# Optimization experiments

Hardware: AMD Instinct MI355X
Metric: run time of the kernel (lower is better)

## Reference

```python
import jax, jax.numpy as jnp
import numpy as np
import math


def setup_inputs() -> dict:
    key = jax.random.key(0)
    ks = jax.random.split(key, 5)
    B, C, E = 4, 2048, 1024
    max_len = 2048
    s = 1.0 / math.sqrt(E)
    return {
        "x": jax.random.normal(ks[0], (B, C, E), dtype=jnp.float32),
        "W_q": jax.random.normal(ks[1], (E, E), dtype=jnp.float32) * s,
        "W_k": jax.random.normal(ks[2], (E, E), dtype=jnp.float32) * s,
        "W_v": jax.random.normal(ks[3], (E, E), dtype=jnp.float32) * s,
        "rel_bias": jax.random.normal(ks[4], (2 * max_len - 1, 1), dtype=jnp.float32),
        "max_len": max_len,
    }


def reference(x, W_q, W_k, W_v, rel_bias, max_len):
    B, C, E = x.shape
    # nn.Linear(bias=False): y = x @ W.T
    Q = jnp.einsum("bce,fe->bcf", x, W_q)
    K = jnp.einsum("bce,fe->bcf", x, W_k)
    V = jnp.einsum("bce,fe->bcf", x, W_v)
    scores = jnp.einsum("bqe,bke->bqk", Q, K) / math.sqrt(E)
    pos = jnp.arange(C)
    rel_dist = jnp.clip(pos[None, :] - pos[:, None] + (max_len - 1), 0, 2 * max_len - 2)
    bias = rel_bias[rel_dist, 0]  # [C, C]
    scores = scores + bias[None, :, :]
    weights = jax.nn.softmax(scores, axis=-1)
    out = jnp.einsum("bqk,bke->bqe", weights, V)
    return out, weights
```

## Files before the change

### kernel.cpp

```cpp
#include <hip/hip_runtime.h>
#include <hip/hip_bf16.h>
#include <math.h>

typedef __attribute__((ext_vector_type(8))) short short8;
typedef __attribute__((ext_vector_type(4))) short short4v;
typedef __attribute__((ext_vector_type(4))) float f32x4;

static __device__ __forceinline__ short f2bf(float f) {
  union { float f; unsigned u; } x;
  x.f = f;
  unsigned r = x.u + 0x7fffu + ((x.u >> 16) & 1u);
  return (short)(r >> 16);
}

#define GLD16(g, l)                                                   \
  __builtin_amdgcn_global_load_lds(                                   \
      (const __attribute__((address_space(1))) void*)(g),             \
      (__attribute__((address_space(3))) void*)(l), 16, 0, 0)
#define BAR() asm volatile("s_barrier" ::: "memory")
#define VMCNT6() asm volatile("s_waitcnt vmcnt(6)" ::: "memory")
#define VMCNT0() asm volatile("s_waitcnt vmcnt(0)" ::: "memory")

__global__ __launch_bounds__(256) void cvt_f32_bf16(const float* __restrict__ in,
                                                    short* __restrict__ out, int n8) {
  int i = blockIdx.x * 256 + threadIdx.x;
  if (i >= n8) return;
  const float4* p = (const float4*)in + (size_t)i * 2;
  float4 a = p[0], b = p[1];
  short8 o;
  o[0] = f2bf(a.x); o[1] = f2bf(a.y); o[2] = f2bf(a.z); o[3] = f2bf(a.w);
  o[4] = f2bf(b.x); o[5] = f2bf(b.y); o[6] = f2bf(b.z); o[7] = f2bf(b.w);
  *((short8*)out + i) = o;
}

template <int MODE>
__global__ __launch_bounds__(512) void gemm3b(
    const short* __restrict__ A, const short* __restrict__ Bt,
    void* __restrict__ C0, void* __restrict__ C1, void* __restrict__ C2,
    const float* __restrict__ rel_bias,
    int N, int K, long aZ, long bZ, long cZ, int Cdim, float scale, int ml) {
  __shared__ short sA[3][256 * 64];
  __shared__ short sB[3][128 * 64];
  const int tid = threadIdx.x, lane = tid & 63, wid = tid >> 6;
  const int z = blockIdx.z;
  const short* Az = A + (size_t)z * aZ;
  const short* Bz = Bt + (size_t)z * bZ;
  const int brow = blockIdx.x * 256, bcol = blockIdx.y * 128;
  const int wr = wid >> 2, wc = wid & 3;
  const int lrow = lane & 15, kg = lane >> 4;
  const int l8 = lane >> 3, lm8 = lane & 7;
  const int scol = (lm8 ^ l8) * 8;

  const short* aS[2][2];
  int aD[2][2];
#pragma unroll
  for (int h = 0; h < 2; ++h)
#pragma unroll
    for (int j = 0; j < 2; ++j) {
      int c = wid * 2 + j;
      int rb = c * 8 + (c >= 8 ? 64 : 0) + h * 64;
      aS[h][j] = Az + (size_t)(brow + rb + l8) * K + scol;
      aD[h][j] = rb * 64;
    }
  const short* bS[2];
  int bD[2];
#pragma unroll
  for (int h = 0; h < 2; ++h) {
    int rb = wid * 8 + h * 64;
    bS[h] = Bz + (size_t)(bcol + rb + l8) * K + scol;
    bD[h] = rb * 64;
  }

  const int sks0 = ((0 + kg) ^ (lrow & 7)) * 8;
  const int sks1 = ((4 + kg) ^ (lrow & 7)) * 8;
  const int aR = (wr * 128 + lrow) * 64;
  const int bR = (wc * 32 + lrow) * 64;

  short8 a[4][2], b[2][2];
  f32x4 acc[8][2] = {};

  short *pa0 = &sA[0][0], *pa1 = &sA[1][0], *pa2 = &sA[2][0];
  short *pb0 = &sB[0][0], *pb1 = &sB[1][0], *pb2 = &sB[2][0];

#define STG_A(PA, H, T)                                          \
  do {                                                           \
    GLD16(aS[H][0] + (size_t)(T) * 64, (PA) + aD[H][0]);         \
    GLD16(aS[H][1] + (size_t)(T) * 64, (PA) + aD[H][1]);         \
  } while (0)
#define STG_B(PB, H, T) GLD16(bS[H] + (size_t)(T) * 64, (PB) + bD[H])
#define RD_A(PA, MH)                                                          \
  do {                                                                        \
    _Pragma("unroll") for (int mq = 0; mq < 4; ++mq) {                        \
      a[mq][0] = *(const short8*)&(PA)[aR + (MH)*4096 + mq * 1024 + sks0];    \
      a[mq][1] = *(const short8*)&(PA)[aR + (MH)*4096 + mq * 1024 + sks1];    \
    }                                                                         \
  } while (0)
#define RD_B(PB)                                                   \
  do {                                                             \
    _Pragma("unroll") for (int nq = 0; nq < 2; ++nq) {             \
      b[nq][0] = *(const short8*)&(PB)[bR + nq * 1024 + sks0];     \
      b[nq][1] = *(const short8*)&(PB)[bR + nq * 1024 + sks1];     \
    }                                                              \
  } while (0)
#define MFMA16(MH)                                                            \
  do {                                                                        \
    __builtin_amdgcn_s_setprio(1);                                            \
    _Pragma("unroll") for (int mq = 0; mq < 4; ++mq)                          \
        _Pragma("unroll") for (int nq = 0; nq < 2; ++nq) {                    \
      acc[(MH)*4 + mq][nq] = __builtin_amdgcn_mfma_f32_16x16x32_bf16(         \
          a[mq][0], b[nq][0], acc[(MH)*4 + mq][nq], 0, 0, 0);                 \
      acc[(MH)*4 + mq][nq] = __builtin_amdgcn_mfma_f32_16x16x32_bf16(         \
          a[mq][1], b[nq][1], acc[(MH)*4 + mq][nq], 0, 0, 0);                 \
    }                                                                         \
    __builtin_amdgcn_s_setprio(0);                                            \
  } while (0)

  STG_A(pa0, 0, 0); STG_B(pb0, 0, 0); STG_A(pa0, 1, 0); STG_B(pb0, 1, 0);
  STG_A(pa1, 0, 1); STG_B(pb1, 0, 1); STG_A(pa1, 1, 1); STG_B(pb1, 1, 1);
  VMCNT6();
  BAR();

  const int NT = K >> 6;
  for (int t = 0; t < NT - 2; ++t) {
    RD_A(pa0, 0); RD_B(pb0);
    STG_A(pa2, 0, t + 2); STG_B(pb2, 0, t + 2);
    BAR();
    MFMA16(0);
    BAR();
    RD_A(pa0, 1);
    STG_A(pa2, 1, t + 2); STG_B(pb2, 1, t + 2);
    VMCNT6();
    BAR();
    MFMA16(1);
    BAR();
    short* q;
    q = pa0; pa0 = pa1; pa1 = pa2; pa2 = q;
    q = pb0; pb0 = pb1; pb1 = pb2; pb2 = q;
  }
  RD_A(pa0, 0); RD_B(pb0);
  BAR(); MFMA16(0); BAR();
  RD_A(pa0, 1);
  VMCNT0();
  BAR(); MFMA16(1); BAR();
  RD_A(pa1, 0); RD_B(pb1);
  BAR(); MFMA16(0); BAR();
  RD_A(pa1, 1);
  BAR(); MFMA16(1);

#pragma unroll
  for (int m = 0; m < 8; ++m) {
#pragma unroll
    for (int n = 0; n < 2; ++n) {
#pragma unroll
      for (int r = 0; r < 4; ++r) {
        float v = acc[m][n][r];
        int gr = brow + wr * 128 + m * 16 + kg * 4 + r;
        int gc = bcol + wc * 32 + n * 16 + lrow;
        if constexpr (MODE == 2) {
          int idx = gc - gr + (ml - 1);
          idx = min(max(idx, 0), 2 * ml - 2);
          ((float*)C0 + (size_t)z * cZ)[(size_t)gr * N + gc] =
              v * scale + rel_bias[idx];
        } else if constexpr (MODE == 3) {
          ((float*)C0 + (size_t)z * cZ)[(size_t)gr * N + gc] = v;
        } else {
          int s = gc >> 10, cc = gc & 1023;
          if (s == 0) {
            ((short*)C0)[(size_t)gr * 1024 + cc] = f2bf(v);
          } else if (s == 1) {
            ((short*)C1)[(size_t)gr * 1024 + cc] = f2bf(v);
          } else {
            int b_ = gr / Cdim, c_ = gr % Cdim;
            ((short*)C2)[((size_t)b_ * 1024 + cc) * Cdim + c_] = f2bf(v);
          }
        }
      }
    }
  }
#undef STG_A
#undef STG_B
#undef RD_A
#undef RD_B
#undef MFMA16
}

__global__ __launch_bounds__(256) void softmax_rows(float* __restrict__ w,
                                                    short* __restrict__ wb, int Cd) {
  const size_t row = blockIdx.x;
  float4* p = (float4*)(w + row * (size_t)Cd);
  const int tid = threadIdx.x;
  float4 v0 = p[tid];
  float4 v1 = p[tid + 256];
  float mx = fmaxf(fmaxf(fmaxf(v0.x, v0.y), fmaxf(v0.z, v0.w)),
                   fmaxf(fmaxf(v1.x, v1.y), fmaxf(v1.z, v1.w)));
#pragma unroll
  for (int o = 32; o; o >>= 1) mx = fmaxf(mx, __shfl_xor(mx, o));
  __shared__ float red[8];
  const int wv = tid >> 6;
  if ((tid & 63) == 0) red[wv] = mx;
  __syncthreads();
  mx = fmaxf(fmaxf(red[0], red[1]), fmaxf(red[2], red[3]));
  v0.x = __expf(v0.x - mx); v0.y = __expf(v0.y - mx);
  v0.z = __expf(v0.z - mx); v0.w = __expf(v0.w - mx);
  v1.x = __expf(v1.x - mx); v1.y = __expf(v1.y - mx);
  v1.z = __expf(v1.z - mx); v1.w = __expf(v1.w - mx);
  float s = v0.x + v0.y + v0.z + v0.w + v1.x + v1.y + v1.z + v1.w;
#pragma unroll
  for (int o = 32; o; o >>= 1) s += __shfl_xor(s, o);
  if ((tid & 63) == 0) red[4 + wv] = s;
  __syncthreads();
  s = red[4] + red[5] + red[6] + red[7];
  float inv = 1.0f / s;
  v0.x *= inv; v0.y *= inv; v0.z *= inv; v0.w *= inv;
  v1.x *= inv; v1.y *= inv; v1.z *= inv; v1.w *= inv;
  p[tid] = v0;
  p[tid + 256] = v1;
  short4v b0, b1;
  b0[0] = f2bf(v0.x); b0[1] = f2bf(v0.y); b0[2] = f2bf(v0.z); b0[3] = f2bf(v0.w);
  b1[0] = f2bf(v1.x); b1[1] = f2bf(v1.y); b1[2] = f2bf(v1.z); b1[3] = f2bf(v1.w);
  short* wrow = wb + row * (size_t)Cd;
  *(short4v*)&wrow[tid * 4] = b0;
  *(short4v*)&wrow[1024 + tid * 4] = b1;
}

extern "C" void kernel_launch(void* const* d_in, const int* in_sizes, int n_in,
                              void* d_out, int out_size, void* d_ws, size_t ws_size,
                              hipStream_t stream) {
  const float* x = (const float*)d_in[0];
  const float* Wq = (const float*)d_in[1];
  const float* Wk = (const float*)d_in[2];
  const float* Wv = (const float*)d_in[3];
  const float* rb = (const float*)d_in[4];

  const int E = 1024;
  const int Mt = in_sizes[0] / E;
  const int Cd = out_size / Mt - E;
  const int B = Mt / Cd;
  const int ml = (in_sizes[4] + 1) / 2;
  const float scale = 1.0f / sqrtf((float)E);

  short* xb = (short*)d_ws;
  short* wqb = xb + (size_t)Mt * E;
  short* wkb = wqb + (size_t)E * E;
  short* wvb = wkb + (size_t)E * E;
  short* Qb = wvb + (size_t)E * E;
  short* Kb = Qb + (size_t)Mt * E;
  short* Vt = Kb + (size_t)Mt * E;
  short* wbf = Qb;

  float* outp = (float*)d_out;
  float* wts = outp + (size_t)Mt * E;

  cvt_f32_bf16<<<(Mt * E) / 2048, 256, 0, stream>>>(x, xb, (Mt * E) / 8);
  cvt_f32_bf16<<<(E * E) / 2048, 256, 0, stream>>>(Wq, wqb, (E * E) / 8);
  cvt_f32_bf16<<<(E * E) / 2048, 256, 0, stream>>>(Wk, wkb, (E * E) / 8);
  cvt_f32_bf16<<<(E * E) / 2048, 256, 0, stream>>>(Wv, wvb, (E * E) / 8);

  dim3 blk(512);
  gemm3b<4><<<dim3(Mt / 256, 3 * E / 128, 1), blk, 0, stream>>>(
      xb, wqb, Qb, Kb, Vt, nullptr, 3 * E, E, 0, 0, 0, Cd, 0.f, ml);
  gemm3b<2><<<dim3(Cd / 256, Cd / 128, B), blk, 0, stream>>>(
      Qb, Kb, wts, nullptr, nullptr, rb, Cd, E, (long)Cd * E, (long)Cd * E,
      (long)Cd * Cd, Cd, scale, ml);
  softmax_rows<<<Mt, 256, 0, stream>>>(wts, wbf, Cd);
  gemm3b<3><<<dim3(Cd / 256, E / 128, B), blk, 0, stream>>>(
      wbf, Vt, outp, nullptr, nullptr, nullptr, E, Cd, (long)Cd * Cd,
      (long)E * Cd, (long)Cd * E, Cd, 0.f, ml);
}
```

Baseline: 209.2 us.

## Enlarge GEMM tiles to 256x256 with K=32 four-stage LDS pipeline

Replaces the 256x128 tile, K=64, three-buffer GEMM with a 256x256 tile, K=32 slice, four-buffer pipeline. Each wave now computes a 128x64 sub-tile of 32 accumulators. This raises MFMA work per LDS read and per global load, and the deeper ring keeps more loads in flight. The larger tile doubles accumulator registers and halves the grid, which may hurt occupancy and wave balance, especially for the smaller output GEMM.

```diff
diff --git a/kernel.cpp b/kernel.cpp
--- a/kernel.cpp
+++ b/kernel.cpp
@@ -18,7 +18,8 @@
       (const __attribute__((address_space(1))) void*)(g),             \
       (__attribute__((address_space(3))) void*)(l), 16, 0, 0)
 #define BAR() asm volatile("s_barrier" ::: "memory")
-#define VMCNT6() asm volatile("s_waitcnt vmcnt(6)" ::: "memory")
+#define VMCNT8() asm volatile("s_waitcnt vmcnt(8)" ::: "memory")
+#define VMCNT4() asm volatile("s_waitcnt vmcnt(4)" ::: "memory")
 #define VMCNT0() asm volatile("s_waitcnt vmcnt(0)" ::: "memory")
 
 __global__ __launch_bounds__(256) void cvt_f32_bf16(const float* __restrict__ in,
@@ -34,128 +35,118 @@
 }
 
 template <int MODE>
-__global__ __launch_bounds__(512) void gemm3b(
+__global__ __launch_bounds__(512) void gemm4b(
     const short* __restrict__ A, const short* __restrict__ Bt,
     void* __restrict__ C0, void* __restrict__ C1, void* __restrict__ C2,
     const float* __restrict__ rel_bias,
     int N, int K, long aZ, long bZ, long cZ, int Cdim, float scale, int ml) {
-  __shared__ short sA[3][256 * 64];
-  __shared__ short sB[3][128 * 64];
+  __shared__ short sA[4][256 * 32];
+  __shared__ short sB[4][256 * 32];
   const int tid = threadIdx.x, lane = tid & 63, wid = tid >> 6;
   const int z = blockIdx.z;
   const short* Az = A + (size_t)z * aZ;
   const short* Bz = Bt + (size_t)z * bZ;
-  const int brow = blockIdx.x * 256, bcol = blockIdx.y * 128;
+  const int brow = blockIdx.x * 256, bcol = blockIdx.y * 256;
   const int wr = wid >> 2, wc = wid & 3;
   const int lrow = lane & 15, kg = lane >> 4;
-  const int l8 = lane >> 3, lm8 = lane & 7;
-  const int scol = (lm8 ^ l8) * 8;
-
-  const short* aS[2][2];
-  int aD[2][2];
-#pragma unroll
-  for (int h = 0; h < 2; ++h)
-#pragma unroll
-    for (int j = 0; j < 2; ++j) {
-      int c = wid * 2 + j;
-      int rb = c * 8 + (c >= 8 ? 64 : 0) + h * 64;
-      aS[h][j] = Az + (size_t)(brow + rb + l8) * K + scol;
-      aD[h][j] = rb * 64;
-    }
-  const short* bS[2];
-  int bD[2];
-#pragma unroll
-  for (int h = 0; h < 2; ++h) {
-    int rb = wid * 8 + h * 64;
-    bS[h] = Bz + (size_t)(bcol + rb + l8) * K + scol;
-    bD[h] = rb * 64;
-  }
-
-  const int sks0 = ((0 + kg) ^ (lrow & 7)) * 8;
-  const int sks1 = ((4 + kg) ^ (lrow & 7)) * 8;
-  const int aR = (wr * 128 + lrow) * 64;
-  const int bR = (wc * 32 + lrow) * 64;
-
-  short8 a[4][2], b[2][2];
-  f32x4 acc[8][2] = {};
-
-  short *pa0 = &sA[0][0], *pa1 = &sA[1][0], *pa2 = &sA[2][0];
-  short *pb0 = &sB[0][0], *pb1 = &sB[1][0], *pb2 = &sB[2][0];
-
-#define STG_A(PA, H, T)                                          \
-  do {                                                           \
-    GLD16(aS[H][0] + (size_t)(T) * 64, (PA) + aD[H][0]);         \
-    GLD16(aS[H][1] + (size_t)(T) * 64, (PA) + aD[H][1]);         \
-  } while (0)
-#define STG_B(PB, H, T) GLD16(bS[H] + (size_t)(T) * 64, (PB) + bD[H])
-#define RD_A(PA, MH)                                                          \
-  do {                                                                        \
-    _Pragma("unroll") for (int mq = 0; mq < 4; ++mq) {                        \
-      a[mq][0] = *(const short8*)&(PA)[aR + (MH)*4096 + mq * 1024 + sks0];    \
-      a[mq][1] = *(const short8*)&(PA)[aR + (MH)*4096 + mq * 1024 + sks1];    \
-    }                                                                         \
-  } while (0)
-#define RD_B(PB)                                                   \
-  do {                                                             \
-    _Pragma("unroll") for (int nq = 0; nq < 2; ++nq) {             \
-      b[nq][0] = *(const short8*)&(PB)[bR + nq * 1024 + sks0];     \
-      b[nq][1] = *(const short8*)&(PB)[bR + nq * 1024 + sks1];     \
-    }                                                              \
+
+  const int srow = wid * 16 + (lane >> 2);
+  const int scol = ((lane & 3) ^ ((lane >> 2) & 3)) * 8;
+  const short* aSrc0 = Az + (size_t)(brow + srow) * K + scol;
+  const short* aSrc1 = Az + (size_t)(brow + 128 + srow) * K + scol;
+  const short* bSrc0 = Bz + (size_t)(bcol + srow) * K + scol;
+  const short* bSrc1 = Bz + (size_t)(bcol + 128 + srow) * K + scol;
+  const int d0 = wid * 512, d1 = 4096 + wid * 512;
+
+  const int kOff = (kg ^ (lrow & 3)) * 8;
+  const int aBase = (wr * 128 + lrow) * 32 + kOff;
+  const int bBase = (wc * 64 + lrow) * 32 + kOff;
+
+  short8 a[4], b[4];
+  f32x4 acc[8][4] = {};
+
+  short *pa0 = &sA[0][0], *pa1 = &sA[1][0], *pa2 = &sA[2][0], *pa3 = &sA[3][0];
+  short *pb0 = &sB[0][0], *pb1 = &sB[1][0], *pb2 = &sB[2][0], *pb3 = &sB[3][0];
+
+#define STG_A(P, T)                                   \
+  do {                                                \
+    GLD16(aSrc0 + (size_t)(T) * 32, (P) + d0);        \
+    GLD16(aSrc1 + (size_t)(T) * 32, (P) + d1);        \
+  } while (0)
+#define STG_B(P, T)                                   \
+  do {                                                \
+    GLD16(bSrc0 + (size_t)(T) * 32, (P) + d0);        \
+    GLD16(bSrc1 + (size_t)(T) * 32, (P) + d1);        \
+  } while (0)
+#define RD_A(P, MH)                                                 \
+  do {                                                              \
+    _Pragma("unroll") for (int m = 0; m < 4; ++m)                   \
+        a[m] = *(const short8*)&(P)[aBase + ((MH)*4 + m) * 512];    \
+  } while (0)
+#define RD_B(P)                                                     \
+  do {                                                              \
+    _Pragma("unroll") for (int n = 0; n < 4; ++n)                   \
+        b[n] = *(const short8*)&(P)[bBase + n * 512];               \
   } while (0)
 #define MFMA16(MH)                                                            \
   do {                                                                        \
     __builtin_amdgcn_s_setprio(1);                                            \
-    _Pragma("unroll") for (int mq = 0; mq < 4; ++mq)                          \
-        _Pragma("unroll") for (int nq = 0; nq < 2; ++nq) {                    \
-      acc[(MH)*4 + mq][nq] = __builtin_amdgcn_mfma_f32_16x16x32_bf16(         \
-          a[mq][0], b[nq][0], acc[(MH)*4 + mq][nq], 0, 0, 0);                 \
-      acc[(MH)*4 + mq][nq] = __builtin_amdgcn_mfma_f32_16x16x32_bf16(         \
-          a[mq][1], b[nq][1], acc[(MH)*4 + mq][nq], 0, 0, 0);                 \
-    }                                                                         \
+    _Pragma("unroll") for (int m = 0; m < 4; ++m)                             \
+        _Pragma("unroll") for (int n = 0; n < 4; ++n)                         \
+            acc[(MH)*4 + m][n] = __builtin_amdgcn_mfma_f32_16x16x32_bf16(     \
+                a[m], b[n], acc[(MH)*4 + m][n], 0, 0, 0);                     \
     __builtin_amdgcn_s_setprio(0);                                            \
   } while (0)
-
-  STG_A(pa0, 0, 0); STG_B(pb0, 0, 0); STG_A(pa0, 1, 0); STG_B(pb0, 1, 0);
-  STG_A(pa1, 0, 1); STG_B(pb1, 0, 1); STG_A(pa1, 1, 1); STG_B(pb1, 1, 1);
-  VMCNT6();
+#define ROT()                                                    \
+  do {                                                           \
+    short* q;                                                    \
+    q = pa0; pa0 = pa1; pa1 = pa2; pa2 = pa3; pa3 = q;           \
+    q = pb0; pb0 = pb1; pb1 = pb2; pb2 = pb3; pb3 = q;           \
+  } while (0)
+
+  STG_A(pa0, 0); STG_B(pb0, 0);
+  STG_A(pa1, 1); STG_B(pb1, 1);
+  STG_A(pa2, 2); STG_B(pb2, 2);
+  VMCNT8();
   BAR();
 
-  const int NT = K >> 6;
-  for (int t = 0; t < NT - 2; ++t) {
+  const int NT = K >> 5;
+  for (int t = 0; t < NT - 3; ++t) {
     RD_A(pa0, 0); RD_B(pb0);
-    STG_A(pa2, 0, t + 2); STG_B(pb2, 0, t + 2);
-    BAR();
-    MFMA16(0);
-    BAR();
+    STG_A(pa3, t + 3);
+    BAR(); MFMA16(0); BAR();
     RD_A(pa0, 1);
-    STG_A(pa2, 1, t + 2); STG_B(pb2, 1, t + 2);
-    VMCNT6();
-    BAR();
-    MFMA16(1);
-    BAR();
-    short* q;
-    q = pa0; pa0 = pa1; pa1 = pa2; pa2 = q;
-    q = pb0; pb0 = pb1; pb1 = pb2; pb2 = q;
+    STG_B(pb3, t + 3);
+    VMCNT8();
+    BAR(); MFMA16(1); BAR();
+    ROT();
   }
+  RD_A(pa0, 0); RD_B(pb0);
+  BAR(); MFMA16(0); BAR();
+  RD_A(pa0, 1);
+  VMCNT4();
+  BAR(); MFMA16(1); BAR();
+  ROT();
   RD_A(pa0, 0); RD_B(pb0);
   BAR(); MFMA16(0); BAR();
   RD_A(pa0, 1);
   VMCNT0();
   BAR(); MFMA16(1); BAR();
-  RD_A(pa1, 0); RD_B(pb1);
+  ROT();
+  RD_A(pa0, 0); RD_B(pb0);
   BAR(); MFMA16(0); BAR();
-  RD_A(pa1, 1);
+  RD_A(pa0, 1);
   BAR(); MFMA16(1);
 
 #pragma unroll
   for (int m = 0; m < 8; ++m) {
 #pragma unroll
-    for (int n = 0; n < 2; ++n) {
+    for (int n = 0; n < 4; ++n) {
 #pragma unroll
       for (int r = 0; r < 4; ++r) {
         float v = acc[m][n][r];
         int gr = brow + wr * 128 + m * 16 + kg * 4 + r;
-        int gc = bcol + wc * 32 + n * 16 + lrow;
+        int gc = bcol + wc * 64 + n * 16 + lrow;
         if constexpr (MODE == 2) {
           int idx = gc - gr + (ml - 1);
           idx = min(max(idx, 0), 2 * ml - 2);
@@ -182,6 +173,7 @@
 #undef RD_A
 #undef RD_B
 #undef MFMA16
+#undef ROT
 }
 
 __global__ __launch_bounds__(256) void softmax_rows(float* __restrict__ w,
@@ -257,13 +249,13 @@
   cvt_f32_bf16<<<(E * E) / 2048, 256, 0, stream>>>(Wv, wvb, (E * E) / 8);
 
   dim3 blk(512);
-  gemm3b<4><<<dim3(Mt / 256, 3 * E / 128, 1), blk, 0, stream>>>(
+  gemm4b<4><<<dim3(Mt / 256, 3 * E / 256, 1), blk, 0, stream>>>(
       xb, wqb, Qb, Kb, Vt, nullptr, 3 * E, E, 0, 0, 0, Cd, 0.f, ml);
-  gemm3b<2><<<dim3(Cd / 256, Cd / 128, B), blk, 0, stream>>>(
+  gemm4b<2><<<dim3(Cd / 256, Cd / 256, B), blk, 0, stream>>>(
       Qb, Kb, wts, nullptr, nullptr, rb, Cd, E, (long)Cd * E, (long)Cd * E,
       (long)Cd * Cd, Cd, scale, ml);
   softmax_rows<<<Mt, 256, 0, stream>>>(wts, wbf, Cd);
-  gemm3b<3><<<dim3(Cd / 256, E / 128, B), blk, 0, stream>>>(
+  gemm4b<3><<<dim3(Cd / 256, E / 256, B), blk, 0, stream>>>(
       wbf, Vt, outp, nullptr, nullptr, nullptr, E, Cd, (long)Cd * Cd,
       (long)E * Cd, (long)Cd * E, Cd, 0.f, ml);
 }
```

After: 251.8 us. +20.4%, slower.

## Enlarge GEMM tiles to 256x256 with double-buffered eight-phase pipeline

Applied to the files above, without the earlier changes.

The GEMM kernel moves from 256x128 output tiles with a triple-buffered 64-deep K pipeline to 256x256 tiles with double-buffered LDS. The K loop processes two 64-wide slices per iteration in eight MFMA phases, interleaving global-to-LDS loads with finer lgkmcnt/vmcnt waits. The goal is higher arithmetic intensity per loaded byte and fewer blocks. The cost is a larger accumulator register footprint (128 floats per lane), more barriers, and fewer blocks, which can hurt occupancy or wave-count balance on the output GEMM (E/256 columns).

```diff
diff --git a/kernel.cpp b/kernel.cpp
--- a/kernel.cpp
+++ b/kernel.cpp
@@ -18,8 +18,10 @@
       (const __attribute__((address_space(1))) void*)(g),             \
       (__attribute__((address_space(3))) void*)(l), 16, 0, 0)
 #define BAR() asm volatile("s_barrier" ::: "memory")
-#define VMCNT6() asm volatile("s_waitcnt vmcnt(6)" ::: "memory")
-#define VMCNT0() asm volatile("s_waitcnt vmcnt(0)" ::: "memory")
+#define LGKM0() asm volatile("s_waitcnt lgkmcnt(0)" ::: "memory")
+#define LGKM8() asm volatile("s_waitcnt lgkmcnt(8)" ::: "memory")
+#define VMC4() asm volatile("s_waitcnt vmcnt(4)" ::: "memory")
+#define VMC0() asm volatile("s_waitcnt vmcnt(0)" ::: "memory")
 
 __global__ __launch_bounds__(256) void cvt_f32_bf16(const float* __restrict__ in,
                                                     short* __restrict__ out, int n8) {
@@ -34,128 +36,149 @@
 }
 
 template <int MODE>
-__global__ __launch_bounds__(512) void gemm3b(
+__global__ __launch_bounds__(512) void gemm8p(
     const short* __restrict__ A, const short* __restrict__ Bt,
     void* __restrict__ C0, void* __restrict__ C1, void* __restrict__ C2,
     const float* __restrict__ rel_bias,
     int N, int K, long aZ, long bZ, long cZ, int Cdim, float scale, int ml) {
-  __shared__ short sA[3][256 * 64];
-  __shared__ short sB[3][128 * 64];
+  __shared__ short sA[2][16384];
+  __shared__ short sB[2][16384];
   const int tid = threadIdx.x, lane = tid & 63, wid = tid >> 6;
   const int z = blockIdx.z;
   const short* Az = A + (size_t)z * aZ;
   const short* Bz = Bt + (size_t)z * bZ;
-  const int brow = blockIdx.x * 256, bcol = blockIdx.y * 128;
+  const int brow = blockIdx.x * 256, bcol = blockIdx.y * 256;
   const int wr = wid >> 2, wc = wid & 3;
   const int lrow = lane & 15, kg = lane >> 4;
-  const int l8 = lane >> 3, lm8 = lane & 7;
-  const int scol = (lm8 ^ l8) * 8;
-
+
+  const int t8 = tid >> 3, t7 = tid & 7;
+  const int logslot = t7 ^ (t8 & 7);
   const short* aS[2][2];
-  int aD[2][2];
+  const short* bS[2][2];
 #pragma unroll
   for (int h = 0; h < 2; ++h)
 #pragma unroll
     for (int j = 0; j < 2; ++j) {
-      int c = wid * 2 + j;
-      int rb = c * 8 + (c >= 8 ? 64 : 0) + h * 64;
-      aS[h][j] = Az + (size_t)(brow + rb + l8) * K + scol;
-      aD[h][j] = rb * 64;
+      aS[h][j] = Az + (size_t)(brow + h * 128 + j * 64 + t8) * K + logslot * 8;
+      bS[h][j] = Bz + (size_t)(bcol + h * 128 + j * 64 + t8) * K + logslot * 8;
     }
-  const short* bS[2];
-  int bD[2];
-#pragma unroll
-  for (int h = 0; h < 2; ++h) {
-    int rb = wid * 8 + h * 64;
-    bS[h] = Bz + (size_t)(bcol + rb + l8) * K + scol;
-    bD[h] = rb * 64;
-  }
-
-  const int sks0 = ((0 + kg) ^ (lrow & 7)) * 8;
-  const int sks1 = ((4 + kg) ^ (lrow & 7)) * 8;
-  const int aR = (wr * 128 + lrow) * 64;
-  const int bR = (wc * 32 + lrow) * 64;
-
-  short8 a[4][2], b[2][2];
-  f32x4 acc[8][2] = {};
-
-  short *pa0 = &sA[0][0], *pa1 = &sA[1][0], *pa2 = &sA[2][0];
-  short *pb0 = &sB[0][0], *pb1 = &sB[1][0], *pb2 = &sB[2][0];
-
-#define STG_A(PA, H, T)                                          \
-  do {                                                           \
-    GLD16(aS[H][0] + (size_t)(T) * 64, (PA) + aD[H][0]);         \
-    GLD16(aS[H][1] + (size_t)(T) * 64, (PA) + aD[H][1]);         \
-  } while (0)
-#define STG_B(PB, H, T) GLD16(bS[H] + (size_t)(T) * 64, (PB) + bD[H])
-#define RD_A(PA, MH)                                                          \
-  do {                                                                        \
-    _Pragma("unroll") for (int mq = 0; mq < 4; ++mq) {                        \
-      a[mq][0] = *(const short8*)&(PA)[aR + (MH)*4096 + mq * 1024 + sks0];    \
-      a[mq][1] = *(const short8*)&(PA)[aR + (MH)*4096 + mq * 1024 + sks1];    \
+
+  const int kOff0 = ((0 + kg) ^ (lrow & 7)) * 8;
+  const int kOff1 = ((4 + kg) ^ (lrow & 7)) * 8;
+  const int rA = (wr * 128 + lrow) * 64;
+  const int rB = (wc * 64 + lrow) * 64;
+
+  short* const A0 = &sA[0][0];
+  short* const A1 = &sA[1][0];
+  short* const B0 = &sB[0][0];
+  short* const B1 = &sB[1][0];
+
+  short8 av[2][2], bv[4][2];
+  f32x4 acc[8][4] = {};
+
+#define STG_A(BUF, H, T)                                                      \
+  do {                                                                        \
+    GLD16(aS[H][0] + (size_t)(T) * 64, &sA[BUF][(H) * 8192 + wid * 512]);     \
+    GLD16(aS[H][1] + (size_t)(T) * 64, &sA[BUF][(H) * 8192 + 4096 + wid * 512]); \
+  } while (0)
+#define STG_B(BUF, H, T)                                                      \
+  do {                                                                        \
+    GLD16(bS[H][0] + (size_t)(T) * 64, &sB[BUF][(H) * 8192 + wid * 512]);     \
+    GLD16(bS[H][1] + (size_t)(T) * 64, &sB[BUF][(H) * 8192 + 4096 + wid * 512]); \
+  } while (0)
+#define RD_APAIR(P, PP)                                                       \
+  do {                                                                        \
+    av[0][0] = *(const short8*)&(P)[rA + ((PP) * 2 + 0) * 1024 + kOff0];      \
+    av[0][1] = *(const short8*)&(P)[rA + ((PP) * 2 + 0) * 1024 + kOff1];      \
+    av[1][0] = *(const short8*)&(P)[rA + ((PP) * 2 + 1) * 1024 + kOff0];      \
+    av[1][1] = *(const short8*)&(P)[rA + ((PP) * 2 + 1) * 1024 + kOff1];      \
+  } while (0)
+#define RD_BALL(P)                                                            \
+  do {                                                                        \
+    _Pragma("unroll") for (int n = 0; n < 4; ++n) {                           \
+      bv[n][0] = *(const short8*)&(P)[rB + n * 1024 + kOff0];                 \
+      bv[n][1] = *(const short8*)&(P)[rB + n * 1024 + kOff1];                 \
     }                                                                         \
   } while (0)
-#define RD_B(PB)                                                   \
-  do {                                                             \
-    _Pragma("unroll") for (int nq = 0; nq < 2; ++nq) {             \
-      b[nq][0] = *(const short8*)&(PB)[bR + nq * 1024 + sks0];     \
-      b[nq][1] = *(const short8*)&(PB)[bR + nq * 1024 + sks1];     \
-    }                                                              \
-  } while (0)
-#define MFMA16(MH)                                                            \
+#define MFMA_PH(PP)                                                           \
   do {                                                                        \
     __builtin_amdgcn_s_setprio(1);                                            \
-    _Pragma("unroll") for (int mq = 0; mq < 4; ++mq)                          \
-        _Pragma("unroll") for (int nq = 0; nq < 2; ++nq) {                    \
-      acc[(MH)*4 + mq][nq] = __builtin_amdgcn_mfma_f32_16x16x32_bf16(         \
-          a[mq][0], b[nq][0], acc[(MH)*4 + mq][nq], 0, 0, 0);                 \
-      acc[(MH)*4 + mq][nq] = __builtin_amdgcn_mfma_f32_16x16x32_bf16(         \
-          a[mq][1], b[nq][1], acc[(MH)*4 + mq][nq], 0, 0, 0);                 \
+    _Pragma("unroll") for (int mp = 0; mp < 2; ++mp)                          \
+        _Pragma("unroll") for (int n = 0; n < 4; ++n) {                       \
+      acc[(PP) * 2 + mp][n] = __builtin_amdgcn_mfma_f32_16x16x32_bf16(        \
+          av[mp][0], bv[n][0], acc[(PP) * 2 + mp][n], 0, 0, 0);               \
+      acc[(PP) * 2 + mp][n] = __builtin_amdgcn_mfma_f32_16x16x32_bf16(        \
+          av[mp][1], bv[n][1], acc[(PP) * 2 + mp][n], 0, 0, 0);               \
     }                                                                         \
     __builtin_amdgcn_s_setprio(0);                                            \
   } while (0)
 
-  STG_A(pa0, 0, 0); STG_B(pb0, 0, 0); STG_A(pa0, 1, 0); STG_B(pb0, 1, 0);
-  STG_A(pa1, 0, 1); STG_B(pb1, 0, 1); STG_A(pa1, 1, 1); STG_B(pb1, 1, 1);
-  VMCNT6();
+  STG_A(0, 0, 0); STG_A(0, 1, 0); STG_B(0, 0, 0); STG_B(0, 1, 0);
+  STG_B(1, 0, 1); STG_B(1, 1, 1);
+  VMC4();
   BAR();
 
-  const int NT = K >> 6;
-  for (int t = 0; t < NT - 2; ++t) {
-    RD_A(pa0, 0); RD_B(pb0);
-    STG_A(pa2, 0, t + 2); STG_B(pb2, 0, t + 2);
+  const int NIT = K >> 7;
+  for (int i = 0; i < NIT - 1; ++i) {
+    const int tU = 2 * i + 1, tV = 2 * i + 2, tW = 2 * i + 3;
+    RD_BALL(B0); RD_APAIR(A0, 0);
+    STG_A(1, 0, tU);
+    LGKM8();
+    BAR(); LGKM0(); MFMA_PH(0); BAR();
+    RD_APAIR(A0, 1); STG_A(1, 1, tU);
+    BAR(); LGKM0(); MFMA_PH(1); BAR();
+    RD_APAIR(A0, 2); STG_B(0, 0, tV);
+    BAR(); LGKM0(); MFMA_PH(2); BAR();
+    RD_APAIR(A0, 3); STG_B(0, 1, tV);
+    BAR(); LGKM0(); MFMA_PH(3);
+    VMC4();
     BAR();
-    MFMA16(0);
+    RD_BALL(B1); RD_APAIR(A1, 0);
+    STG_A(0, 0, tV);
+    LGKM8();
+    BAR(); LGKM0(); MFMA_PH(0); BAR();
+    RD_APAIR(A1, 1); STG_A(0, 1, tV);
+    BAR(); LGKM0(); MFMA_PH(1); BAR();
+    RD_APAIR(A1, 2); STG_B(1, 0, tW);
+    BAR(); LGKM0(); MFMA_PH(2); BAR();
+    RD_APAIR(A1, 3); STG_B(1, 1, tW);
+    BAR(); LGKM0(); MFMA_PH(3);
+    VMC4();
     BAR();
-    RD_A(pa0, 1);
-    STG_A(pa2, 1, t + 2); STG_B(pb2, 1, t + 2);
-    VMCNT6();
+  }
+  {
+    const int tU = 2 * NIT - 1;
+    RD_BALL(B0); RD_APAIR(A0, 0);
+    STG_A(1, 0, tU);
+    LGKM8();
+    BAR(); LGKM0(); MFMA_PH(0); BAR();
+    RD_APAIR(A0, 1); STG_A(1, 1, tU);
+    BAR(); LGKM0(); MFMA_PH(1); BAR();
+    RD_APAIR(A0, 2);
+    BAR(); LGKM0(); MFMA_PH(2); BAR();
+    RD_APAIR(A0, 3);
+    BAR(); LGKM0(); MFMA_PH(3);
+    VMC0();
     BAR();
-    MFMA16(1);
-    BAR();
-    short* q;
-    q = pa0; pa0 = pa1; pa1 = pa2; pa2 = q;
-    q = pb0; pb0 = pb1; pb1 = pb2; pb2 = q;
+    RD_BALL(B1); RD_APAIR(A1, 0);
+    BAR(); LGKM0(); MFMA_PH(0); BAR();
+    RD_APAIR(A1, 1);
+    BAR(); LGKM0(); MFMA_PH(1); BAR();
+    RD_APAIR(A1, 2);
+    BAR(); LGKM0(); MFMA_PH(2); BAR();
+    RD_APAIR(A1, 3);
+    BAR(); LGKM0(); MFMA_PH(3);
   }
-  RD_A(pa0, 0); RD_B(pb0);
-  BAR(); MFMA16(0); BAR();
-  RD_A(pa0, 1);
-  VMCNT0();
-  BAR(); MFMA16(1); BAR();
-  RD_A(pa1, 0); RD_B(pb1);
-  BAR(); MFMA16(0); BAR();
-  RD_A(pa1, 1);
-  BAR(); MFMA16(1);
 
 #pragma unroll
   for (int m = 0; m < 8; ++m) {
 #pragma unroll
-    for (int n = 0; n < 2; ++n) {
+    for (int n = 0; n < 4; ++n) {
 #pragma unroll
       for (int r = 0; r < 4; ++r) {
         float v = acc[m][n][r];
         int gr = brow + wr * 128 + m * 16 + kg * 4 + r;
-        int gc = bcol + wc * 32 + n * 16 + lrow;
+        int gc = bcol + wc * 64 + n * 16 + lrow;
         if constexpr (MODE == 2) {
           int idx = gc - gr + (ml - 1);
           idx = min(max(idx, 0), 2 * ml - 2);
@@ -179,9 +202,9 @@
   }
 #undef STG_A
 #undef STG_B
-#undef RD_A
-#undef RD_B
-#undef MFMA16
+#undef RD_APAIR
+#undef RD_BALL
+#undef MFMA_PH
 }
 
 __global__ __launch_bounds__(256) void softmax_rows(float* __restrict__ w,
@@ -257,13 +280,13 @@
   cvt_f32_bf16<<<(E * E) / 2048, 256, 0, stream>>>(Wv, wvb, (E * E) / 8);
 
   dim3 blk(512);
-  gemm3b<4><<<dim3(Mt / 256, 3 * E / 128, 1), blk, 0, stream>>>(
+  gemm8p<4><<<dim3(Mt / 256, 3 * E / 256, 1), blk, 0, stream>>>(
       xb, wqb, Qb, Kb, Vt, nullptr, 3 * E, E, 0, 0, 0, Cd, 0.f, ml);
-  gemm3b<2><<<dim3(Cd / 256, Cd / 128, B), blk, 0, stream>>>(
+  gemm8p<2><<<dim3(Cd / 256, Cd / 256, B), blk, 0, stream>>>(
       Qb, Kb, wts, nullptr, nullptr, rb, Cd, E, (long)Cd * E, (long)Cd * E,
       (long)Cd * Cd, Cd, scale, ml);
   softmax_rows<<<Mt, 256, 0, stream>>>(wts, wbf, Cd);
-  gemm3b<3><<<dim3(Cd / 256, E / 128, B), blk, 0, stream>>>(
+  gemm8p<3><<<dim3(Cd / 256, E / 256, B), blk, 0, stream>>>(
       wbf, Vt, outp, nullptr, nullptr, nullptr, E, Cd, (long)Cd * Cd,
       (long)E * Cd, (long)Cd * E, Cd, 0.f, ml);
 }
```

After: 241.7 us. 15.6% more time.
